# Kernel tuning notes

Hardware: AMD Instinct MI355X
Metric: run time of the kernel (lower is better)

Reference implementation:

```python
import jax, jax.numpy as jnp
import numpy as np

FEATURE_SIZE = 1_000_000
FIELD_SIZE = 39
EMBED_SIZE = 32
HIDDEN = [400, 400]
BATCH = 16384


def setup_inputs() -> dict:
    key = jax.random.key(0)
    ks = jax.random.split(key, 10)
    p_emb = 1.0 / np.sqrt(FEATURE_SIZE + EMBED_SIZE)
    p_bias = 1.0 / np.sqrt(FEATURE_SIZE + 1)
    d_in = FIELD_SIZE * EMBED_SIZE
    p1 = 1.0 / np.sqrt(d_in + HIDDEN[0])
    p2 = 1.0 / np.sqrt(HIDDEN[0] + HIDDEN[1])
    d_cat = FIELD_SIZE + EMBED_SIZE + HIDDEN[-1]
    pf = 1.0 / np.sqrt(d_cat + 1)
    return {
        "feat_index": jax.random.randint(ks[0], (BATCH, FIELD_SIZE), 0, FEATURE_SIZE),
        "feat_value": jax.random.uniform(ks[1], (BATCH, FIELD_SIZE), dtype=jnp.float32),
        "feature_embedding": jax.random.uniform(ks[2], (FEATURE_SIZE, EMBED_SIZE), jnp.float32, -p_emb, p_emb),
        "feature_bias": jax.random.uniform(ks[3], (FEATURE_SIZE, 1), jnp.float32, -p_bias, p_bias),
        "W1": jax.random.uniform(ks[4], (HIDDEN[0], d_in), jnp.float32, -p1, p1),
        "b1": jnp.zeros((HIDDEN[0],), jnp.float32),
        "W2": jax.random.uniform(ks[5], (HIDDEN[1], HIDDEN[0]), jnp.float32, -p2, p2),
        "b2": jnp.zeros((HIDDEN[1],), jnp.float32),
        "final_W": jax.random.uniform(ks[6], (1, d_cat), jnp.float32, -pf, pf),
        "final_b": jnp.zeros((1,), jnp.float32),
    }


def reference(feat_index, feat_value, feature_embedding, feature_bias,
              W1, b1, W2, b2, final_W, final_b):
    B = feat_index.shape[0]
    fv = feat_value[:, :, None]                          # [B, F, 1]
    emb = feature_embedding[feat_index] * fv             # [B, F, E]

    # first-order FM term: [B, F]
    first_order = jnp.sum(feature_bias[feat_index] * fv, axis=-1)

    # second-order FM term: 0.5 * ((sum e)^2 - sum e^2), [B, E]
    sum_emb = jnp.sum(emb, axis=1)
    second_order = 0.5 * (sum_emb * sum_emb - jnp.sum(emb * emb, axis=1))

    # deep component
    deep_y = emb.reshape(B, FIELD_SIZE * EMBED_SIZE)
    deep_y = jax.nn.relu(deep_y @ W1.T + b1)
    deep_y = jax.nn.relu(deep_y @ W2.T + b2)

    concat_input = jnp.concatenate([first_order, second_order, deep_y], axis=1)
    output = concat_input @ final_W.T + final_b          # [B, 1]
    return (output, first_order, second_order, deep_y)
```

## Files before the change

kernel.cpp:

```cpp
#include <hip/hip_runtime.h>
#include <hip/hip_bf16.h>

#define BATCH 16384
#define FIELD 39
#define EMB 32
#define DIN (FIELD * EMB)
#define HID 400
#define NPAD 512
#define K2P 416

typedef __attribute__((ext_vector_type(8))) short short8;
typedef __attribute__((ext_vector_type(4))) float float4v;

static __device__ __forceinline__ unsigned short f2bf(float f) {
    __hip_bfloat16 h = __float2bfloat16(f);
    return *(unsigned short*)&h;
}

__global__ __launch_bounds__(256) void gather_fm_kernel(
    const int* __restrict__ feat_index,
    const float* __restrict__ feat_value,
    const float* __restrict__ emb_table,
    const float* __restrict__ bias_table,
    unsigned short* __restrict__ emb_ws,
    float* __restrict__ first_order,
    float* __restrict__ second_order)
{
    const int lane = threadIdx.x & 63;
    const int wave = threadIdx.x >> 6;
    const int r = blockIdx.x * 4 + wave;

    int   idx0 = 0;
    float val0 = 0.f;
    if (lane < FIELD) {
        idx0 = feat_index[r * FIELD + lane];
        val0 = feat_value[r * FIELD + lane];
        first_order[r * FIELD + lane] = bias_table[idx0] * val0;
    }

    const int fsub = lane >> 3;
    const int j4   = (lane & 7) * 4;

    float sx = 0.f, sy = 0.f, sz = 0.f, sw = 0.f;
    float qx = 0.f, qy = 0.f, qz = 0.f, qw = 0.f;

    #pragma unroll
    for (int step = 0; step < 5; ++step) {
        const int  f  = step * 8 + fsub;
        const int  fi = __shfl(idx0, f, 64);
        const float fv = __shfl(val0, f, 64);
        const bool ok = (f < FIELD);
        float4 e4 = make_float4(0.f, 0.f, 0.f, 0.f);
        if (ok) {
            float4 t = *(const float4*)(emb_table + (size_t)fi * EMB + j4);
            e4.x = t.x * fv; e4.y = t.y * fv; e4.z = t.z * fv; e4.w = t.w * fv;
            uint2 pk;
            pk.x = (unsigned)f2bf(e4.x) | ((unsigned)f2bf(e4.y) << 16);
            pk.y = (unsigned)f2bf(e4.z) | ((unsigned)f2bf(e4.w) << 16);
            *(uint2*)(emb_ws + (size_t)r * DIN + step * 256 + lane * 4) = pk;
        }
        sx += e4.x; sy += e4.y; sz += e4.z; sw += e4.w;
        qx += e4.x * e4.x; qy += e4.y * e4.y; qz += e4.z * e4.z; qw += e4.w * e4.w;
    }

    #pragma unroll
    for (int d = 8; d < 64; d <<= 1) {
        sx += __shfl_xor(sx, d, 64); sy += __shfl_xor(sy, d, 64);
        sz += __shfl_xor(sz, d, 64); sw += __shfl_xor(sw, d, 64);
        qx += __shfl_xor(qx, d, 64); qy += __shfl_xor(qy, d, 64);
        qz += __shfl_xor(qz, d, 64); qw += __shfl_xor(qw, d, 64);
    }

    if (lane < 8) {
        float4 so4;
        so4.x = 0.5f * (sx * sx - qx);
        so4.y = 0.5f * (sy * sy - qy);
        so4.z = 0.5f * (sz * sz - qz);
        so4.w = 0.5f * (sw * sw - qw);
        *(float4*)(second_order + (size_t)r * EMB + lane * 4) = so4;
    }
}

__global__ __launch_bounds__(256) void cvt_weights(
    const float* __restrict__ W1, const float* __restrict__ W2,
    const float* __restrict__ b1, const float* __restrict__ b2,
    unsigned short* __restrict__ W1b, unsigned short* __restrict__ W2b,
    float* __restrict__ b1p, float* __restrict__ b2p)
{
    const int n1p = NPAD * DIN;
    const int n2p = NPAD * K2P;
    int i = blockIdx.x * 256 + threadIdx.x;
    if (i < n1p) {
        int row = i / DIN, col = i - row * DIN;
        W1b[i] = (row < HID) ? f2bf(W1[row * DIN + col]) : (unsigned short)0;
    } else if (i < n1p + n2p) {
        int j = i - n1p;
        int row = j / K2P, col = j - row * K2P;
        W2b[j] = (row < HID && col < HID) ? f2bf(W2[row * HID + col]) : (unsigned short)0;
    } else if (i < n1p + n2p + NPAD) {
        int k = i - n1p - n2p;
        b1p[k] = (k < HID) ? b1[k] : 0.f;
    } else if (i < n1p + n2p + 2 * NPAD) {
        int k = i - n1p - n2p - NPAD;
        b2p[k] = (k < HID) ? b2[k] : 0.f;
    }
}

template<bool OUT_BF16>
__global__ __launch_bounds__(256) void gemm_mfma_gll(
    const unsigned short* __restrict__ A, int lda,
    const unsigned short* __restrict__ Bw, int ldb,
    const float* __restrict__ bias,
    void* __restrict__ Cp, int ldc, int stn,
    int K)
{
    constexpr int BM = 128, BN = 128, BK = 32;
    __shared__ __align__(16) unsigned short As[BM][BK];
    __shared__ __align__(16) unsigned short Bs[BN][BK];

    const int tid  = threadIdx.x;
    const int wave = tid >> 6;
    const int lane = tid & 63;
    const int quad = lane >> 4;
    const int l16  = lane & 15;
    const int wm = (wave & 1) * 64;
    const int wn = (wave >> 1) * 64;
    const int m0 = blockIdx.x * BM;
    const int n0 = blockIdx.y * BN;

    const int sr   = lane >> 2;
    const int slot = lane & 3;

    float4v acc[4][4];
    #pragma unroll
    for (int i = 0; i < 4; ++i)
        #pragma unroll
        for (int j = 0; j < 4; ++j)
            acc[i][j] = (float4v)(0.f);

    const int fslot = (quad ^ (l16 & 3)) * 8;

    for (int k0 = 0; k0 < K; k0 += BK) {
        #pragma unroll
        for (int p = 0; p < 2; ++p) {
            const int seg = wave * 2 + p;
            const int r   = seg * 16 + sr;
            const int c   = slot ^ (r & 3);
            const unsigned short* gA = A + (size_t)(m0 + r) * lda + k0 + c * 8;
            unsigned short* lA = &As[0][0] + seg * 512 + lane * 8;
            __builtin_amdgcn_global_load_lds(
                (const __attribute__((address_space(1))) unsigned int*)gA,
                (__attribute__((address_space(3))) unsigned int*)lA, 16, 0, 0);
            const unsigned short* gB = Bw + (size_t)(n0 + r) * ldb + k0 + c * 8;
            unsigned short* lB = &Bs[0][0] + seg * 512 + lane * 8;
            __builtin_amdgcn_global_load_lds(
                (const __attribute__((address_space(1))) unsigned int*)gB,
                (__attribute__((address_space(3))) unsigned int*)lB, 16, 0, 0);
        }
        __syncthreads();

        short8 af[4], bf[4];
        #pragma unroll
        for (int i = 0; i < 4; ++i)
            af[i] = *(const short8*)(&As[wm + i * 16 + l16][fslot]);
        #pragma unroll
        for (int j = 0; j < 4; ++j)
            bf[j] = *(const short8*)(&Bs[wn + j * 16 + l16][fslot]);

        #pragma unroll
        for (int i = 0; i < 4; ++i)
            #pragma unroll
            for (int j = 0; j < 4; ++j)
                acc[i][j] = __builtin_amdgcn_mfma_f32_16x16x32_bf16(
                    af[i], bf[j], acc[i][j], 0, 0, 0);
        __syncthreads();
    }

    #pragma unroll
    for (int i = 0; i < 4; ++i) {
        const int rbase = m0 + wm + i * 16 + quad * 4;
        #pragma unroll
        for (int j = 0; j < 4; ++j) {
            const int col = n0 + wn + j * 16 + l16;
            if (col < stn) {
                const float bv = bias[col];
                #pragma unroll
                for (int r2 = 0; r2 < 4; ++r2) {
                    float v = acc[i][j][r2] + bv;
                    v = v > 0.f ? v : 0.f;
                    if (OUT_BF16)
                        ((unsigned short*)Cp)[(size_t)(rbase + r2) * ldc + col] = f2bf(v);
                    else
                        ((float*)Cp)[(size_t)(rbase + r2) * ldc + col] = v;
                }
            }
        }
    }
}

__global__ __launch_bounds__(256) void final_kernel(
    const float* __restrict__ fo,
    const float* __restrict__ so,
    const float* __restrict__ dy,
    const float* __restrict__ fW,
    const float* __restrict__ fb,
    float* __restrict__ out)
{
    const int lane = threadIdx.x & 63;
    const int wave = threadIdx.x >> 6;
    const int r = blockIdx.x * 4 + wave;

    float s = 0.f;
    if (lane < FIELD)
        s += fo[(size_t)r * FIELD + lane] * fW[lane];
    if (lane < EMB)
        s += so[(size_t)r * EMB + lane] * fW[FIELD + lane];
    for (int e = lane; e < HID; e += 64)
        s += dy[(size_t)r * HID + e] * fW[FIELD + EMB + e];

    #pragma unroll
    for (int off = 32; off > 0; off >>= 1)
        s += __shfl_down(s, off, 64);

    if (lane == 0)
        out[r] = s + fb[0];
}

extern "C" void kernel_launch(void* const* d_in, const int* in_sizes, int n_in,
                              void* d_out, int out_size, void* d_ws, size_t ws_size,
                              hipStream_t stream)
{
    const int*   feat_index = (const int*)d_in[0];
    const float* feat_value = (const float*)d_in[1];
    const float* emb_table  = (const float*)d_in[2];
    const float* bias_table = (const float*)d_in[3];
    const float* W1         = (const float*)d_in[4];
    const float* b1         = (const float*)d_in[5];
    const float* W2         = (const float*)d_in[6];
    const float* b2         = (const float*)d_in[7];
    const float* fW         = (const float*)d_in[8];
    const float* fb         = (const float*)d_in[9];

    float* out = (float*)d_out;
    float* out0 = out;
    float* fo   = out + BATCH;
    float* so   = out + (size_t)BATCH * (1 + FIELD);
    float* dy   = out + (size_t)BATCH * (1 + FIELD + EMB);

    unsigned short* emb_ws = (unsigned short*)d_ws;
    unsigned short* h1     = emb_ws + (size_t)BATCH * DIN;
    unsigned short* W1b    = h1 + (size_t)BATCH * K2P;
    unsigned short* W2b    = W1b + (size_t)NPAD * DIN;
    float*          b1p    = (float*)(W2b + (size_t)NPAD * K2P);
    float*          b2p    = b1p + NPAD;

    const int ncvt = NPAD * DIN + NPAD * K2P + 2 * NPAD;
    cvt_weights<<<(ncvt + 255) / 256, 256, 0, stream>>>(
        W1, W2, b1, b2, W1b, W2b, b1p, b2p);

    gather_fm_kernel<<<BATCH / 4, 256, 0, stream>>>(
        feat_index, feat_value, emb_table, bias_table, emb_ws, fo, so);

    dim3 grid_g(BATCH / 128, NPAD / 128);
    gemm_mfma_gll<true ><<<grid_g, 256, 0, stream>>>(
        emb_ws, DIN, W1b, DIN, b1p, h1, K2P, K2P, DIN);
    gemm_mfma_gll<false><<<grid_g, 256, 0, stream>>>(
        h1, K2P, W2b, K2P, b2p, dy, HID, HID, K2P);

    final_kernel<<<BATCH / 4, 256, 0, stream>>>(fo, so, dy, fW, fb, out0);
}
```

Baseline: 278.2 us.

## Merge gather and weight prep, fold final dot into GEMM2, widen BK to 64

Weight conversion and the embedding gather/FM step now run in one launch. The first- and second-order parts of the final dot product are computed in that prep kernel. The deep part is reduced in the epilogue of the second GEMM and added to the output with atomicAdd, which removes the separate final kernel. The GEMM k-tile grows from 32 to 64 with a new XOR swizzle, and K is padded to 1280 and 448 so it divides evenly. The cost is extra zero-padding work and a dependence on the atomic ordering, since the prep kernel must write out0 before GEMM2 adds into it.

```diff
diff --git a/kernel.cpp b/kernel.cpp
--- a/kernel.cpp
+++ b/kernel.cpp
@@ -4,10 +4,11 @@
 #define BATCH 16384
 #define FIELD 39
 #define EMB 32
-#define DIN (FIELD * EMB)
+#define DIN 1248
+#define K1P 1280
 #define HID 400
+#define K2P 448
 #define NPAD 512
-#define K2P 416
 
 typedef __attribute__((ext_vector_type(8))) short short8;
 typedef __attribute__((ext_vector_type(4))) float float4v;
@@ -17,106 +18,131 @@
     return *(unsigned short*)&h;
 }
 
-__global__ __launch_bounds__(256) void gather_fm_kernel(
+#define CVT_ELEMS (NPAD * K1P + NPAD * K2P + 2 * NPAD)
+#define GATHER_BLOCKS (BATCH / 4)
+
+__global__ __launch_bounds__(256) void prep_kernel(
     const int* __restrict__ feat_index,
     const float* __restrict__ feat_value,
     const float* __restrict__ emb_table,
     const float* __restrict__ bias_table,
+    const float* __restrict__ W1, const float* __restrict__ b1,
+    const float* __restrict__ W2, const float* __restrict__ b2,
+    const float* __restrict__ fW, const float* __restrict__ fb,
     unsigned short* __restrict__ emb_ws,
+    unsigned short* __restrict__ W1b,
+    unsigned short* __restrict__ W2b,
+    float* __restrict__ b1p, float* __restrict__ b2p,
     float* __restrict__ first_order,
-    float* __restrict__ second_order)
+    float* __restrict__ second_order,
+    float* __restrict__ out0)
 {
-    const int lane = threadIdx.x & 63;
-    const int wave = threadIdx.x >> 6;
-    const int r = blockIdx.x * 4 + wave;
-
-    int   idx0 = 0;
-    float val0 = 0.f;
-    if (lane < FIELD) {
-        idx0 = feat_index[r * FIELD + lane];
-        val0 = feat_value[r * FIELD + lane];
-        first_order[r * FIELD + lane] = bias_table[idx0] * val0;
-    }
-
-    const int fsub = lane >> 3;
-    const int j4   = (lane & 7) * 4;
-
-    float sx = 0.f, sy = 0.f, sz = 0.f, sw = 0.f;
-    float qx = 0.f, qy = 0.f, qz = 0.f, qw = 0.f;
-
-    #pragma unroll
-    for (int step = 0; step < 5; ++step) {
-        const int  f  = step * 8 + fsub;
-        const int  fi = __shfl(idx0, f, 64);
-        const float fv = __shfl(val0, f, 64);
-        const bool ok = (f < FIELD);
-        float4 e4 = make_float4(0.f, 0.f, 0.f, 0.f);
-        if (ok) {
-            float4 t = *(const float4*)(emb_table + (size_t)fi * EMB + j4);
-            e4.x = t.x * fv; e4.y = t.y * fv; e4.z = t.z * fv; e4.w = t.w * fv;
-            uint2 pk;
-            pk.x = (unsigned)f2bf(e4.x) | ((unsigned)f2bf(e4.y) << 16);
-            pk.y = (unsigned)f2bf(e4.z) | ((unsigned)f2bf(e4.w) << 16);
-            *(uint2*)(emb_ws + (size_t)r * DIN + step * 256 + lane * 4) = pk;
-        }
-        sx += e4.x; sy += e4.y; sz += e4.z; sw += e4.w;
-        qx += e4.x * e4.x; qy += e4.y * e4.y; qz += e4.z * e4.z; qw += e4.w * e4.w;
-    }
-
-    #pragma unroll
-    for (int d = 8; d < 64; d <<= 1) {
-        sx += __shfl_xor(sx, d, 64); sy += __shfl_xor(sy, d, 64);
-        sz += __shfl_xor(sz, d, 64); sw += __shfl_xor(sw, d, 64);
-        qx += __shfl_xor(qx, d, 64); qy += __shfl_xor(qy, d, 64);
-        qz += __shfl_xor(qz, d, 64); qw += __shfl_xor(qw, d, 64);
-    }
-
-    if (lane < 8) {
-        float4 so4;
-        so4.x = 0.5f * (sx * sx - qx);
-        so4.y = 0.5f * (sy * sy - qy);
-        so4.z = 0.5f * (sz * sz - qz);
-        so4.w = 0.5f * (sw * sw - qw);
-        *(float4*)(second_order + (size_t)r * EMB + lane * 4) = so4;
-    }
-}
-
-__global__ __launch_bounds__(256) void cvt_weights(
-    const float* __restrict__ W1, const float* __restrict__ W2,
-    const float* __restrict__ b1, const float* __restrict__ b2,
-    unsigned short* __restrict__ W1b, unsigned short* __restrict__ W2b,
-    float* __restrict__ b1p, float* __restrict__ b2p)
-{
-    const int n1p = NPAD * DIN;
-    const int n2p = NPAD * K2P;
-    int i = blockIdx.x * 256 + threadIdx.x;
-    if (i < n1p) {
-        int row = i / DIN, col = i - row * DIN;
-        W1b[i] = (row < HID) ? f2bf(W1[row * DIN + col]) : (unsigned short)0;
-    } else if (i < n1p + n2p) {
-        int j = i - n1p;
-        int row = j / K2P, col = j - row * K2P;
-        W2b[j] = (row < HID && col < HID) ? f2bf(W2[row * HID + col]) : (unsigned short)0;
-    } else if (i < n1p + n2p + NPAD) {
-        int k = i - n1p - n2p;
-        b1p[k] = (k < HID) ? b1[k] : 0.f;
-    } else if (i < n1p + n2p + 2 * NPAD) {
-        int k = i - n1p - n2p - NPAD;
-        b2p[k] = (k < HID) ? b2[k] : 0.f;
-    }
-}
-
-template<bool OUT_BF16>
-__global__ __launch_bounds__(256) void gemm_mfma_gll(
+    if (blockIdx.x < GATHER_BLOCKS) {
+        const int lane = threadIdx.x & 63;
+        const int wave = threadIdx.x >> 6;
+        const int r = blockIdx.x * 4 + wave;
+
+        int   idx0 = 0;
+        float val0 = 0.f;
+        float s1 = 0.f;
+        if (lane < FIELD) {
+            idx0 = feat_index[r * FIELD + lane];
+            val0 = feat_value[r * FIELD + lane];
+            float fov = bias_table[idx0] * val0;
+            first_order[r * FIELD + lane] = fov;
+            s1 = fov * fW[lane];
+        }
+
+        const int fsub = lane >> 3;
+        const int j4   = (lane & 7) * 4;
+
+        float sx = 0.f, sy = 0.f, sz = 0.f, sw = 0.f;
+        float qx = 0.f, qy = 0.f, qz = 0.f, qw = 0.f;
+
+        #pragma unroll
+        for (int step = 0; step < 5; ++step) {
+            const int   f  = step * 8 + fsub;
+            const int   fi = __shfl(idx0, f, 64);
+            const float fv = __shfl(val0, f, 64);
+            float4 e4 = make_float4(0.f, 0.f, 0.f, 0.f);
+            if (f < FIELD) {
+                float4 t = *(const float4*)(emb_table + (size_t)fi * EMB + j4);
+                e4.x = t.x * fv; e4.y = t.y * fv; e4.z = t.z * fv; e4.w = t.w * fv;
+                uint2 pk;
+                pk.x = (unsigned)f2bf(e4.x) | ((unsigned)f2bf(e4.y) << 16);
+                pk.y = (unsigned)f2bf(e4.z) | ((unsigned)f2bf(e4.w) << 16);
+                *(uint2*)(emb_ws + (size_t)r * K1P + step * 256 + lane * 4) = pk;
+            }
+            sx += e4.x; sy += e4.y; sz += e4.z; sw += e4.w;
+            qx += e4.x * e4.x; qy += e4.y * e4.y; qz += e4.z * e4.z; qw += e4.w * e4.w;
+        }
+
+        if (lane < 8) {
+            uint2 z; z.x = 0u; z.y = 0u;
+            *(uint2*)(emb_ws + (size_t)r * K1P + DIN + lane * 4) = z;
+        }
+
+        #pragma unroll
+        for (int d = 8; d < 64; d <<= 1) {
+            sx += __shfl_xor(sx, d, 64); sy += __shfl_xor(sy, d, 64);
+            sz += __shfl_xor(sz, d, 64); sw += __shfl_xor(sw, d, 64);
+            qx += __shfl_xor(qx, d, 64); qy += __shfl_xor(qy, d, 64);
+            qz += __shfl_xor(qz, d, 64); qw += __shfl_xor(qw, d, 64);
+        }
+
+        float s2 = 0.f;
+        if (lane < 8) {
+            float4 so4;
+            so4.x = 0.5f * (sx * sx - qx);
+            so4.y = 0.5f * (sy * sy - qy);
+            so4.z = 0.5f * (sz * sz - qz);
+            so4.w = 0.5f * (sw * sw - qw);
+            *(float4*)(second_order + (size_t)r * EMB + lane * 4) = so4;
+            const float* fw = fW + FIELD + lane * 4;
+            s2 = so4.x * fw[0] + so4.y * fw[1] + so4.z * fw[2] + so4.w * fw[3];
+        }
+
+        float s = s1 + s2;
+        #pragma unroll
+        for (int d = 1; d < 64; d <<= 1)
+            s += __shfl_xor(s, d, 64);
+        if (lane == 0)
+            out0[r] = s + fb[0];
+    } else {
+        int i = (blockIdx.x - GATHER_BLOCKS) * 256 + threadIdx.x;
+        const int n1p = NPAD * K1P;
+        const int n2p = NPAD * K2P;
+        if (i < n1p) {
+            int row = i / K1P, col = i - row * K1P;
+            W1b[i] = (row < HID && col < DIN)
+                   ? f2bf(W1[row * DIN + col]) : (unsigned short)0;
+        } else if (i < n1p + n2p) {
+            int j = i - n1p;
+            int row = j / K2P, col = j - row * K2P;
+            W2b[j] = (row < HID && col < HID)
+                   ? f2bf(W2[row * HID + col]) : (unsigned short)0;
+        } else if (i < n1p + n2p + NPAD) {
+            int k = i - n1p - n2p;
+            b1p[k] = (k < HID) ? b1[k] : 0.f;
+        } else if (i < n1p + n2p + 2 * NPAD) {
+            int k = i - n1p - n2p - NPAD;
+            b2p[k] = (k < HID) ? b2[k] : 0.f;
+        }
+    }
+}
+
+template<bool OUT_BF16, bool FINAL_DOT>
+__global__ __launch_bounds__(256) void gemm_mfma(
     const unsigned short* __restrict__ A, int lda,
     const unsigned short* __restrict__ Bw, int ldb,
     const float* __restrict__ bias,
-    void* __restrict__ Cp, int ldc, int stn,
-    int K)
+    void* __restrict__ Cp, int ldc, int stn, int K,
+    const float* __restrict__ fW, float* __restrict__ out0)
 {
-    constexpr int BM = 128, BN = 128, BK = 32;
-    __shared__ __align__(16) unsigned short As[BM][BK];
-    __shared__ __align__(16) unsigned short Bs[BN][BK];
+    constexpr int BM = 128, BN = 128, BK = 64;
+    __shared__ __align__(16) unsigned short As[BM * BK];
+    __shared__ __align__(16) unsigned short Bs[BN * BK];
+    __shared__ float part[2][BM];
 
     const int tid  = threadIdx.x;
     const int wave = tid >> 6;
@@ -128,8 +154,8 @@
     const int m0 = blockIdx.x * BM;
     const int n0 = blockIdx.y * BN;
 
-    const int sr   = lane >> 2;
-    const int slot = lane & 3;
+    const int lrow8 = lane >> 3;
+    const int cg    = (lane & 7) ^ lrow8;
 
     float4v acc[4][4];
     #pragma unroll
@@ -138,41 +164,42 @@
         for (int j = 0; j < 4; ++j)
             acc[i][j] = (float4v)(0.f);
 
-    const int fslot = (quad ^ (l16 & 3)) * 8;
-
     for (int k0 = 0; k0 < K; k0 += BK) {
         #pragma unroll
-        for (int p = 0; p < 2; ++p) {
-            const int seg = wave * 2 + p;
-            const int r   = seg * 16 + sr;
-            const int c   = slot ^ (r & 3);
-            const unsigned short* gA = A + (size_t)(m0 + r) * lda + k0 + c * 8;
-            unsigned short* lA = &As[0][0] + seg * 512 + lane * 8;
+        for (int p = 0; p < 4; ++p) {
+            const int seg = wave * 4 + p;
+            const int r   = seg * 8 + lrow8;
+            const unsigned short* gA = A + (size_t)(m0 + r) * lda + k0 + cg * 8;
+            unsigned short* lA = As + seg * 512 + lane * 8;
             __builtin_amdgcn_global_load_lds(
                 (const __attribute__((address_space(1))) unsigned int*)gA,
                 (__attribute__((address_space(3))) unsigned int*)lA, 16, 0, 0);
-            const unsigned short* gB = Bw + (size_t)(n0 + r) * ldb + k0 + c * 8;
-            unsigned short* lB = &Bs[0][0] + seg * 512 + lane * 8;
+            const unsigned short* gB = Bw + (size_t)(n0 + r) * ldb + k0 + cg * 8;
+            unsigned short* lB = Bs + seg * 512 + lane * 8;
             __builtin_amdgcn_global_load_lds(
                 (const __attribute__((address_space(1))) unsigned int*)gB,
                 (__attribute__((address_space(3))) unsigned int*)lB, 16, 0, 0);
         }
         __syncthreads();
 
-        short8 af[4], bf[4];
-        #pragma unroll
-        for (int i = 0; i < 4; ++i)
-            af[i] = *(const short8*)(&As[wm + i * 16 + l16][fslot]);
-        #pragma unroll
-        for (int j = 0; j < 4; ++j)
-            bf[j] = *(const short8*)(&Bs[wn + j * 16 + l16][fslot]);
-
-        #pragma unroll
-        for (int i = 0; i < 4; ++i)
+        #pragma unroll
+        for (int s = 0; s < 2; ++s) {
+            short8 af[4], bf[4];
+            #pragma unroll
+            for (int i = 0; i < 4; ++i)
+                af[i] = *(const short8*)(As + (wm + i * 16 + l16) * 64
+                                            + (((s * 4 + quad) ^ (l16 & 7)) * 8));
             #pragma unroll
             for (int j = 0; j < 4; ++j)
-                acc[i][j] = __builtin_amdgcn_mfma_f32_16x16x32_bf16(
-                    af[i], bf[j], acc[i][j], 0, 0, 0);
+                bf[j] = *(const short8*)(Bs + (wn + j * 16 + l16) * 64
+                                            + (((s * 4 + quad) ^ (l16 & 7)) * 8));
+            #pragma unroll
+            for (int i = 0; i < 4; ++i)
+                #pragma unroll
+                for (int j = 0; j < 4; ++j)
+                    acc[i][j] = __builtin_amdgcn_mfma_f32_16x16x32_bf16(
+                        af[i], bf[j], acc[i][j], 0, 0, 0);
+        }
         __syncthreads();
     }
 
@@ -188,42 +215,41 @@
                 for (int r2 = 0; r2 < 4; ++r2) {
                     float v = acc[i][j][r2] + bv;
                     v = v > 0.f ? v : 0.f;
+                    acc[i][j][r2] = v;
                     if (OUT_BF16)
                         ((unsigned short*)Cp)[(size_t)(rbase + r2) * ldc + col] = f2bf(v);
                     else
                         ((float*)Cp)[(size_t)(rbase + r2) * ldc + col] = v;
                 }
+            } else {
+                #pragma unroll
+                for (int r2 = 0; r2 < 4; ++r2) acc[i][j][r2] = 0.f;
             }
         }
     }
-}
-
-__global__ __launch_bounds__(256) void final_kernel(
-    const float* __restrict__ fo,
-    const float* __restrict__ so,
-    const float* __restrict__ dy,
-    const float* __restrict__ fW,
-    const float* __restrict__ fb,
-    float* __restrict__ out)
-{
-    const int lane = threadIdx.x & 63;
-    const int wave = threadIdx.x >> 6;
-    const int r = blockIdx.x * 4 + wave;
-
-    float s = 0.f;
-    if (lane < FIELD)
-        s += fo[(size_t)r * FIELD + lane] * fW[lane];
-    if (lane < EMB)
-        s += so[(size_t)r * EMB + lane] * fW[FIELD + lane];
-    for (int e = lane; e < HID; e += 64)
-        s += dy[(size_t)r * HID + e] * fW[FIELD + EMB + e];
-
-    #pragma unroll
-    for (int off = 32; off > 0; off >>= 1)
-        s += __shfl_down(s, off, 64);
-
-    if (lane == 0)
-        out[r] = s + fb[0];
+
+    if (FINAL_DOT) {
+        #pragma unroll
+        for (int i = 0; i < 4; ++i) {
+            #pragma unroll
+            for (int r2 = 0; r2 < 4; ++r2) {
+                float s = 0.f;
+                #pragma unroll
+                for (int j = 0; j < 4; ++j) {
+                    const int col = n0 + wn + j * 16 + l16;
+                    const float fwv = (col < HID) ? fW[FIELD + EMB + col] : 0.f;
+                    s = fmaf(acc[i][j][r2], fwv, s);
+                }
+                s += __shfl_xor(s, 1, 64); s += __shfl_xor(s, 2, 64);
+                s += __shfl_xor(s, 4, 64); s += __shfl_xor(s, 8, 64);
+                if (l16 == 0)
+                    part[wn >> 6][wm + i * 16 + quad * 4 + r2] = s;
+            }
+        }
+        __syncthreads();
+        if (tid < BM)
+            atomicAdd(out0 + m0 + tid, part[0][tid] + part[1][tid]);
+    }
 }
 
 extern "C" void kernel_launch(void* const* d_in, const int* in_sizes, int n_in,
@@ -248,24 +274,21 @@
     float* dy   = out + (size_t)BATCH * (1 + FIELD + EMB);
 
     unsigned short* emb_ws = (unsigned short*)d_ws;
-    unsigned short* h1     = emb_ws + (size_t)BATCH * DIN;
+    unsigned short* h1     = emb_ws + (size_t)BATCH * K1P;
     unsigned short* W1b    = h1 + (size_t)BATCH * K2P;
-    unsigned short* W2b    = W1b + (size_t)NPAD * DIN;
+    unsigned short* W2b    = W1b + (size_t)NPAD * K1P;
     float*          b1p    = (float*)(W2b + (size_t)NPAD * K2P);
     float*          b2p    = b1p + NPAD;
 
-    const int ncvt = NPAD * DIN + NPAD * K2P + 2 * NPAD;
-    cvt_weights<<<(ncvt + 255) / 256, 256, 0, stream>>>(
-        W1, W2, b1, b2, W1b, W2b, b1p, b2p);
-
-    gather_fm_kernel<<<BATCH / 4, 256, 0, stream>>>(
-        feat_index, feat_value, emb_table, bias_table, emb_ws, fo, so);
+    const int cvt_blocks = (CVT_ELEMS + 255) / 256;
+    prep_kernel<<<GATHER_BLOCKS + cvt_blocks, 256, 0, stream>>>(
+        feat_index, feat_value, emb_table, bias_table,
+        W1, b1, W2, b2, fW, fb,
+        emb_ws, W1b, W2b, b1p, b2p, fo, so, out0);
 
     dim3 grid_g(BATCH / 128, NPAD / 128);
-    gemm_mfma_gll<true ><<<grid_g, 256, 0, stream>>>(
-        emb_ws, DIN, W1b, DIN, b1p, h1, K2P, K2P, DIN);
-    gemm_mfma_gll<false><<<grid_g, 256, 0, stream>>>(
-        h1, K2P, W2b, K2P, b2p, dy, HID, HID, K2P);
-
-    final_kernel<<<BATCH / 4, 256, 0, stream>>>(fo, so, dy, fW, fb, out0);
-}
+    gemm_mfma<true, false><<<grid_g, 256, 0, stream>>>(
+        emb_ws, K1P, W1b, K1P, b1p, h1, K2P, K2P, K1P, nullptr, nullptr);
+    gemm_mfma<false, true><<<grid_g, 256, 0, stream>>>(
+        h1, K2P, W2b, K2P, b2p, dy, HID, HID, K2P, fW, out0);
+}
```

New measurement: 267.3 us. 3.9% less time.
